# Performance work log

Measured on AMD Instinct MI355X. Metric: run time of the kernel, lower is better.

The kernel has to match this reference:

```python
import jax, jax.numpy as jnp
import numpy as np

EPS = 1e-5  # torch LayerNorm default


def _ln(x, w, b):
    m = jnp.mean(x, axis=-1, keepdims=True)
    v = jnp.mean((x - m) ** 2, axis=-1, keepdims=True)
    return (x - m) / jnp.sqrt(v + EPS) * w + b


def _conv1x1(x, w, b):
    # x: [B,C,H,W], w: [O,C], b: [O]
    return jnp.einsum('bchw,oc->bohw', x, w) + b[None, :, None, None]


def setup_inputs() -> dict:
    key = jax.random.key(0)
    ks = jax.random.split(key, 5)
    B, Cin, H, W = 8, 384, 64, 64
    D, N = 128, 512
    s = lambda k, shape, scale=0.02: jax.random.normal(k, shape, jnp.float32) * scale
    return {
        'x': jax.random.normal(ks[0], (B, Cin, H, W), jnp.float32),
        'DR': jax.random.normal(ks[1], (N, D), jnp.float32),
        'conv_in_w': s(ks[2], (D, Cin)),
        'conv_in_b': jnp.zeros((D,), jnp.float32),
        'sem_w': s(ks[3], (D, D)),
        'sem_b': jnp.zeros((D,), jnp.float32),
        'norm1_w': jnp.ones((D,), jnp.float32),
        'norm1_b': jnp.zeros((D,), jnp.float32),
        'norm2_w': jnp.ones((D,), jnp.float32),
        'norm2_b': jnp.zeros((D,), jnp.float32),
        'conv_out_w': s(ks[4], (Cin, D)),
        'conv_out_b': jnp.zeros((Cin,), jnp.float32),
    }


def reference(x, DR, conv_in_w, conv_in_b, sem_w, sem_b, norm1_w, norm1_b,
              norm2_w, norm2_b, conv_out_w, conv_out_b):
    B, _, H, W = x.shape
    N = DR.shape[0]
    x_align = _conv1x1(x, conv_in_w, conv_in_b)                      # [B,D,H,W]
    x_sem = _conv1x1(x_align, sem_w, sem_b)                          # semantic_extra (1x1 conv)
    x_sem = x_sem.transpose(0, 2, 3, 1).reshape(B, H * W, -1)        # [B,HW,D]
    x_sem = _ln(x_sem, norm1_w, norm1_b)
    dr = _ln(DR, norm2_w, norm2_b).T                                 # [D,N] (same for all batches)
    # NOTE: original applies norm_1 TWICE for the numerator (faithful quirk)
    c_u = jnp.einsum('bld,dn->bln', _ln(x_sem, norm1_w, norm1_b), dr)  # [B,HW,N]
    c_d_l = jnp.sqrt(jnp.sum(x_sem ** 2, axis=-1, keepdims=True))      # [B,HW,1]
    c_d_r = jnp.sqrt(jnp.sum(dr ** 2, axis=0, keepdims=True))[None]    # [1,1,N]
    sim = c_u / (c_d_l * c_d_r)
    sim_soft = jax.nn.softmax(sim, axis=-1)                          # [B,HW,N]
    sim2d = sim_soft.transpose(0, 2, 1).reshape(B, N, H, W)
    degrad = jnp.einsum('bln,dn->bdl', sim_soft, dr).reshape(B, -1, H, W)  # [B,D,H,W]
    # pow-mask with per-batch min-max normalization
    mask_v = jnp.max(sim2d ** 3, axis=1, keepdims=True)              # [B,1,H,W]
    mn = jnp.min(mask_v.reshape(B, -1), axis=1).reshape(B, 1, 1, 1)
    mx = jnp.max(mask_v.reshape(B, -1), axis=1).reshape(B, 1, 1, 1)
    mask_v = 1.0 - (mask_v - mn) / (mx - mn)
    # topk row selection (torch fancy indexing gives [B,B,K,N]; squeeze(1) is a no-op for B>1)
    max_values = jnp.max(sim_soft, axis=2)                           # [B,HW]
    K = (H * W) // 50
    _, top_idx = jax.lax.top_k(max_values, K)                        # [B,K]
    results = jnp.take(sim_soft, top_idx, axis=1)                    # [B,B,K,N]
    out_img = _conv1x1(degrad, conv_out_w, conv_out_b)               # [B,Cin,H,W]
    return (mask_v, out_img, results)
```

## Files before the change

kernel.cpp:

```cpp
#include <hip/hip_runtime.h>
#include <cstdint>

#define EPS 1e-5f
#define BB   8
#define CIN  384
#define HWs  4096
#define LT   32768
#define DD   128
#define NN   512
#define TOPK 81

typedef short short8 __attribute__((ext_vector_type(8)));
typedef float f32x4  __attribute__((ext_vector_type(4)));

__device__ __forceinline__ unsigned short f2bf(float x) {
  unsigned u = __float_as_uint(x);
  u += 0x7fffu + ((u >> 16) & 1u);
  return (unsigned short)(u >> 16);
}
__device__ __forceinline__ float bf2f(unsigned u16) {
  return __uint_as_float(u16 << 16);
}
__device__ __forceinline__ void put_frag(unsigned short* buf, int tile, int rc, int k, float v) {
  int ks = k >> 5, g = (k >> 3) & 3, j = k & 7;
  int basehw = ((tile * 4 + ks) * 2) * 512 + (g * 16 + rc) * 8 + j;
  unsigned short hi = f2bf(v);
  buf[basehw] = hi;
  buf[basehw + 512] = f2bf(v - bf2f(hi));
}

__global__ __launch_bounds__(64) void k_dr(const float* __restrict__ DR,
    const float* __restrict__ w2, const float* __restrict__ b2,
    const float* __restrict__ w1, const float* __restrict__ b1,
    unsigned short* __restrict__ drwF, unsigned short* __restrict__ drlnF,
    float* __restrict__ t2, float* __restrict__ rcr) {
  int n = blockIdx.x;
  int lane = threadIdx.x;
  const float* row = DR + n * DD;
  float x0 = row[lane], x1 = row[lane + 64];
  float s = x0 + x1, sq = x0 * x0 + x1 * x1;
  #pragma unroll
  for (int o = 32; o; o >>= 1) { s += __shfl_xor(s, o); sq += __shfl_xor(sq, o); }
  float m = s * (1.f / 128.f);
  float v = sq * (1.f / 128.f) - m * m;
  float inv = rsqrtf(v + EPS);
  float y0 = (x0 - m) * inv * w2[lane] + b2[lane];
  float y1 = (x1 - m) * inv * w2[lane + 64] + b2[lane + 64];
  int nt = n >> 4, cc = n & 15;
  put_frag(drwF, nt, cc, lane, y0 * w1[lane]);
  put_frag(drwF, nt, cc, lane + 64, y1 * w1[lane + 64]);
  int ks = n >> 5, gB = (n >> 3) & 3, j = n & 7;
  {
    int d = lane;
    unsigned short hi = f2bf(y0);
    int base = (((d >> 4) * 16 + ks) * 2) * 512 + (gB * 16 + (d & 15)) * 8 + j;
    drlnF[base] = hi;
    drlnF[base + 512] = f2bf(y0 - bf2f(hi));
  }
  {
    int d = lane + 64;
    unsigned short hi = f2bf(y1);
    int base = (((d >> 4) * 16 + ks) * 2) * 512 + (gB * 16 + (d & 15)) * 8 + j;
    drlnF[base] = hi;
    drlnF[base + 512] = f2bf(y1 - bf2f(hi));
  }
  float pt2 = y0 * b1[lane] + y1 * b1[lane + 64];
  float pss = y0 * y0 + y1 * y1;
  #pragma unroll
  for (int o = 32; o; o >>= 1) { pt2 += __shfl_xor(pt2, o); pss += __shfl_xor(pss, o); }
  if (lane == 0) { t2[n] = pt2; rcr[n] = rsqrtf(pss); }
}

__global__ __launch_bounds__(256) void k_bprep(const float* __restrict__ src,
                                               unsigned short* __restrict__ dst,
                                               int K) {
  int rt = blockIdx.x, kb = blockIdx.y;
  int t = threadIdx.x, m = t >> 4, kg = t & 15;
  int k0 = kb * 128 + kg * 8;
  const float* s = src + (size_t)(rt * 16 + m) * K + k0;
  float4 f0 = *(const float4*)s;
  float4 f1 = *(const float4*)(s + 4);
  float vs[8] = {f0.x, f0.y, f0.z, f0.w, f1.x, f1.y, f1.z, f1.w};
  short8 hi, lo;
  #pragma unroll
  for (int j = 0; j < 8; ++j) {
    unsigned short h = f2bf(vs[j]);
    hi[j] = (short)h;
    lo[j] = (short)f2bf(vs[j] - bf2f(h));
  }
  int nkt = K >> 5;
  int ks = k0 >> 5, g = (k0 >> 3) & 3;
  short8* D8 = (short8*)dst;
  int base = ((rt * nkt + ks) * 2) * 64 + g * 16 + m;
  D8[base] = hi;
  D8[base + 64] = lo;
}

__global__ __launch_bounds__(256) void k_convin(const float* __restrict__ x,
    const unsigned short* __restrict__ WinF, const float* __restrict__ bias,
    unsigned short* __restrict__ xaF) {
  __shared__ float smem[64 * 132];
  int t = threadIdx.x;
  int w = t >> 6, lane = t & 63, m = lane & 15, g = lane >> 4;
  int l0 = blockIdx.x * 64;
  int b = l0 >> 12, hw0 = l0 & 4095;
  const float* xb = x + (size_t)b * CIN * HWs + hw0;
  const short8* B8 = (const short8*)WinF;
  f32x4 acc[4][2];
  #pragma unroll
  for (int lt = 0; lt < 4; ++lt)
    #pragma unroll
    for (int j2 = 0; j2 < 2; ++j2) acc[lt][j2] = (f32x4){0.f, 0.f, 0.f, 0.f};
  for (int ks = 0; ks < 12; ++ks) {
    short8 ah[4], al[4];
    const float* xc = xb + (size_t)(ks * 32 + g * 8) * HWs;
    #pragma unroll
    for (int lt = 0; lt < 4; ++lt) {
      const float* xcl = xc + lt * 16 + m;
      float v[8];
      #pragma unroll
      for (int j = 0; j < 8; ++j) v[j] = xcl[(size_t)j * HWs];
      #pragma unroll
      for (int j = 0; j < 8; ++j) {
        unsigned short h = f2bf(v[j]);
        ah[lt][j] = (short)h;
        al[lt][j] = (short)f2bf(v[j] - bf2f(h));
      }
    }
    #pragma unroll
    for (int j2 = 0; j2 < 2; ++j2) {
      int dt = w * 2 + j2;
      short8 bh = B8[((dt * 12 + ks) * 2 + 0) * 64 + lane];
      short8 bl = B8[((dt * 12 + ks) * 2 + 1) * 64 + lane];
      #pragma unroll
      for (int lt = 0; lt < 4; ++lt) {
        acc[lt][j2] = __builtin_amdgcn_mfma_f32_16x16x32_bf16(ah[lt], bh, acc[lt][j2], 0, 0, 0);
        acc[lt][j2] = __builtin_amdgcn_mfma_f32_16x16x32_bf16(ah[lt], bl, acc[lt][j2], 0, 0, 0);
        acc[lt][j2] = __builtin_amdgcn_mfma_f32_16x16x32_bf16(al[lt], bh, acc[lt][j2], 0, 0, 0);
      }
    }
  }
  float bia[2] = {bias[w * 32 + m], bias[w * 32 + 16 + m]};
  #pragma unroll
  for (int lt = 0; lt < 4; ++lt)
    #pragma unroll
    for (int j2 = 0; j2 < 2; ++j2)
      #pragma unroll
      for (int r = 0; r < 4; ++r)
        smem[(lt * 16 + g * 4 + r) * 132 + (w * 2 + j2) * 16 + m] = acc[lt][j2][r] + bia[j2];
  __syncthreads();
  short8* X8 = (short8*)xaF;
  #pragma unroll
  for (int it = 0; it < 4; ++it) {
    int idx = it * 256 + t;
    int l = idx & 63, dq = idx >> 6;
    const float* src = &smem[l * 132 + dq * 8];
    float4 f0 = *(const float4*)src;
    float4 f1 = *(const float4*)(src + 4);
    float vs[8] = {f0.x, f0.y, f0.z, f0.w, f1.x, f1.y, f1.z, f1.w};
    short8 hi, lo;
    #pragma unroll
    for (int j = 0; j < 8; ++j) {
      unsigned short h = f2bf(vs[j]);
      hi[j] = (short)h;
      lo[j] = (short)f2bf(vs[j] - bf2f(h));
    }
    int ltg = (l0 + l) >> 4;
    int idx8 = ((ltg * 4 + (dq >> 2)) * 2) * 64 + (dq & 3) * 16 + (l & 15);
    X8[idx8] = hi;
    X8[idx8 + 64] = lo;
  }
}

__global__ __launch_bounds__(256) void k_sem(const unsigned short* __restrict__ xaF,
    const unsigned short* __restrict__ semWF, const float* __restrict__ bias,
    const float* __restrict__ w1, const float* __restrict__ b1,
    unsigned short* __restrict__ ApF, float* __restrict__ rclv) {
  __shared__ float smem[64 * 132];
  __shared__ float sredS[64][4], sredQ[64][4];
  __shared__ float rowM[64], rowI[64];
  int t = threadIdx.x;
  int w = t >> 6, lane = t & 63, m = lane & 15, g = lane >> 4;
  int l0 = blockIdx.x * 64;
  int lt0 = l0 >> 4;
  const short8* A8 = (const short8*)xaF;
  const short8* B8 = (const short8*)semWF;
  f32x4 acc[4][2];
  #pragma unroll
  for (int lt = 0; lt < 4; ++lt)
    #pragma unroll
    for (int j2 = 0; j2 < 2; ++j2) acc[lt][j2] = (f32x4){0.f, 0.f, 0.f, 0.f};
  #pragma unroll
  for (int ks = 0; ks < 4; ++ks) {
    short8 ah[4], al[4];
    #pragma unroll
    for (int lt = 0; lt < 4; ++lt) {
      ah[lt] = A8[(((lt0 + lt) * 4 + ks) * 2 + 0) * 64 + lane];
      al[lt] = A8[(((lt0 + lt) * 4 + ks) * 2 + 1) * 64 + lane];
    }
    #pragma unroll
    for (int j2 = 0; j2 < 2; ++j2) {
      int dt = w * 2 + j2;
      short8 bh = B8[((dt * 4 + ks) * 2 + 0) * 64 + lane];
      short8 bl = B8[((dt * 4 + ks) * 2 + 1) * 64 + lane];
      #pragma unroll
      for (int lt = 0; lt < 4; ++lt) {
        acc[lt][j2] = __builtin_amdgcn_mfma_f32_16x16x32_bf16(ah[lt], bh, acc[lt][j2], 0, 0, 0);
        acc[lt][j2] = __builtin_amdgcn_mfma_f32_16x16x32_bf16(ah[lt], bl, acc[lt][j2], 0, 0, 0);
        acc[lt][j2] = __builtin_amdgcn_mfma_f32_16x16x32_bf16(al[lt], bh, acc[lt][j2], 0, 0, 0);
      }
    }
  }
  float bia[2] = {bias[w * 32 + m], bias[w * 32 + 16 + m]};
  #pragma unroll
  for (int lt = 0; lt < 4; ++lt)
    #pragma unroll
    for (int j2 = 0; j2 < 2; ++j2)
      #pragma unroll
      for (int r = 0; r < 4; ++r) acc[lt][j2][r] += bia[j2];
  float s1[4][4], q1[4][4];
  #pragma unroll
  for (int lt = 0; lt < 4; ++lt)
    #pragma unroll
    for (int r = 0; r < 4; ++r) {
      float a = acc[lt][0][r], b2v = acc[lt][1][r];
      s1[lt][r] = a + b2v;
      q1[lt][r] = a * a + b2v * b2v;
    }
  #pragma unroll
  for (int o = 1; o < 16; o <<= 1)
    #pragma unroll
    for (int lt = 0; lt < 4; ++lt)
      #pragma unroll
      for (int r = 0; r < 4; ++r) {
        s1[lt][r] += __shfl_xor(s1[lt][r], o);
        q1[lt][r] += __shfl_xor(q1[lt][r], o);
      }
  if (m == 0) {
    #pragma unroll
    for (int lt = 0; lt < 4; ++lt)
      #pragma unroll
      for (int r = 0; r < 4; ++r) {
        sredS[lt * 16 + g * 4 + r][w] = s1[lt][r];
        sredQ[lt * 16 + g * 4 + r][w] = q1[lt][r];
      }
  }
  __syncthreads();
  if (t < 64) {
    float S = sredS[t][0] + sredS[t][1] + sredS[t][2] + sredS[t][3];
    float Q = sredQ[t][0] + sredQ[t][1] + sredQ[t][2] + sredQ[t][3];
    float mu = S * (1.f / 128.f);
    float var = Q * (1.f / 128.f) - mu * mu;
    rowM[t] = mu;
    rowI[t] = rsqrtf(var + EPS);
  }
  __syncthreads();
  float w1v[2] = {w1[w * 32 + m], w1[w * 32 + 16 + m]};
  float b1v[2] = {b1[w * 32 + m], b1[w * 32 + 16 + m]};
  #pragma unroll
  for (int lt = 0; lt < 4; ++lt)
    #pragma unroll
    for (int r = 0; r < 4; ++r) {
      float mu = rowM[lt * 16 + g * 4 + r];
      float iv = rowI[lt * 16 + g * 4 + r];
      float y0 = (acc[lt][0][r] - mu) * iv * w1v[0] + b1v[0];
      float y1 = (acc[lt][1][r] - mu) * iv * w1v[1] + b1v[1];
      acc[lt][0][r] = y0; acc[lt][1][r] = y1;
      s1[lt][r] = y0 + y1;
      q1[lt][r] = y0 * y0 + y1 * y1;
    }
  #pragma unroll
  for (int o = 1; o < 16; o <<= 1)
    #pragma unroll
    for (int lt = 0; lt < 4; ++lt)
      #pragma unroll
      for (int r = 0; r < 4; ++r) {
        s1[lt][r] += __shfl_xor(s1[lt][r], o);
        q1[lt][r] += __shfl_xor(q1[lt][r], o);
      }
  if (m == 0) {
    #pragma unroll
    for (int lt = 0; lt < 4; ++lt)
      #pragma unroll
      for (int r = 0; r < 4; ++r) {
        sredS[lt * 16 + g * 4 + r][w] = s1[lt][r];
        sredQ[lt * 16 + g * 4 + r][w] = q1[lt][r];
      }
  }
  __syncthreads();
  if (t < 64) {
    float S = sredS[t][0] + sredS[t][1] + sredS[t][2] + sredS[t][3];
    float Q = sredQ[t][0] + sredQ[t][1] + sredQ[t][2] + sredQ[t][3];
    float m2 = S * (1.f / 128.f);
    float v2 = Q * (1.f / 128.f) - m2 * m2;
    float inv2 = rsqrtf(v2 + EPS);
    float rcl = rsqrtf(Q);
    rowM[t] = m2;
    rowI[t] = inv2 * rcl;
    rclv[l0 + t] = rcl;
  }
  __syncthreads();
  #pragma unroll
  for (int lt = 0; lt < 4; ++lt)
    #pragma unroll
    for (int r = 0; r < 4; ++r) {
      float m2 = rowM[lt * 16 + g * 4 + r];
      float sc = rowI[lt * 16 + g * 4 + r];
      smem[(lt * 16 + g * 4 + r) * 132 + w * 32 + m] = (acc[lt][0][r] - m2) * sc;
      smem[(lt * 16 + g * 4 + r) * 132 + w * 32 + 16 + m] = (acc[lt][1][r] - m2) * sc;
    }
  __syncthreads();
  short8* O8 = (short8*)ApF;
  #pragma unroll
  for (int it = 0; it < 4; ++it) {
    int idx = it * 256 + t;
    int l = idx & 63, dq = idx >> 6;
    const float* src = &smem[l * 132 + dq * 8];
    float4 f0 = *(const float4*)src;
    float4 f1 = *(const float4*)(src + 4);
    float vs[8] = {f0.x, f0.y, f0.z, f0.w, f1.x, f1.y, f1.z, f1.w};
    short8 hi, lo;
    #pragma unroll
    for (int j = 0; j < 8; ++j) {
      unsigned short h = f2bf(vs[j]);
      hi[j] = (short)h;
      lo[j] = (short)f2bf(vs[j] - bf2f(h));
    }
    int ltg = (l0 + l) >> 4;
    int idx8 = ((ltg * 4 + (dq >> 2)) * 2) * 64 + (dq & 3) * 16 + (l & 15);
    O8[idx8] = hi;
    O8[idx8 + 64] = lo;
  }
}

__global__ __launch_bounds__(256) void k_scores(const unsigned short* __restrict__ ApF,
    const unsigned short* __restrict__ drwF, const float* __restrict__ t2g,
    const float* __restrict__ rcrg, const float* __restrict__ rclg,
    unsigned short* __restrict__ pF, float* __restrict__ maxv) {
  __shared__ __align__(16) float sredM[32][4];
  __shared__ __align__(16) float sredS[32][4];
  __shared__ __align__(16) unsigned short plds[32 * 520];
  int t = threadIdx.x;
  int w = t >> 6, lane = t & 63, c = lane & 15, g = lane >> 4;
  int l0 = blockIdx.x * 32;
  int lt0 = blockIdx.x * 2;
  const short8* A8 = (const short8*)ApF;
  const short8* B8 = (const short8*)drwF;
  f32x4 acc[2][8];
  #pragma unroll
  for (int il = 0; il < 2; ++il)
    #pragma unroll
    for (int jn = 0; jn < 8; ++jn) acc[il][jn] = (f32x4){0.f, 0.f, 0.f, 0.f};
  #pragma unroll
  for (int ks = 0; ks < 4; ++ks) {
    short8 ah0 = A8[((lt0 * 4 + ks) * 2 + 0) * 64 + lane];
    short8 al0 = A8[((lt0 * 4 + ks) * 2 + 1) * 64 + lane];
    short8 ah1 = A8[(((lt0 + 1) * 4 + ks) * 2 + 0) * 64 + lane];
    short8 al1 = A8[(((lt0 + 1) * 4 + ks) * 2 + 1) * 64 + lane];
    #pragma unroll
    for (int jn = 0; jn < 8; ++jn) {
      int nt = w * 8 + jn;
      short8 bh = B8[((nt * 4 + ks) * 2 + 0) * 64 + lane];
      short8 bl = B8[((nt * 4 + ks) * 2 + 1) * 64 + lane];
      acc[0][jn] = __builtin_amdgcn_mfma_f32_16x16x32_bf16(ah0, bh, acc[0][jn], 0, 0, 0);
      acc[0][jn] = __builtin_amdgcn_mfma_f32_16x16x32_bf16(ah0, bl, acc[0][jn], 0, 0, 0);
      acc[0][jn] = __builtin_amdgcn_mfma_f32_16x16x32_bf16(al0, bh, acc[0][jn], 0, 0, 0);
      acc[1][jn] = __builtin_amdgcn_mfma_f32_16x16x32_bf16(ah1, bh, acc[1][jn], 0, 0, 0);
      acc[1][jn] = __builtin_amdgcn_mfma_f32_16x16x32_bf16(ah1, bl, acc[1][jn], 0, 0, 0);
      acc[1][jn] = __builtin_amdgcn_mfma_f32_16x16x32_bf16(al1, bh, acc[1][jn], 0, 0, 0);
    }
  }
  float rcrv[8], t2v[8];
  #pragma unroll
  for (int jn = 0; jn < 8; ++jn) {
    int n = w * 128 + jn * 16 + c;
    rcrv[jn] = rcrg[n]; t2v[jn] = t2g[n];
  }
  float rclr[2][4];
  #pragma unroll
  for (int il = 0; il < 2; ++il)
    #pragma unroll
    for (int r = 0; r < 4; ++r)
      rclr[il][r] = rclg[l0 + il * 16 + g * 4 + r];
  float M[2][4];
  #pragma unroll
  for (int il = 0; il < 2; ++il)
    #pragma unroll
    for (int r = 0; r < 4; ++r) M[il][r] = -1e30f;
  #pragma unroll
  for (int il = 0; il < 2; ++il)
    #pragma unroll
    for (int jn = 0; jn < 8; ++jn) {
      f32x4 a = acc[il][jn];
      #pragma unroll
      for (int r = 0; r < 4; ++r) {
        float s = rcrv[jn] * (a[r] + rclr[il][r] * t2v[jn]);
        a[r] = s;
        M[il][r] = fmaxf(M[il][r], s);
      }
      acc[il][jn] = a;
    }
  #pragma unroll
  for (int o = 1; o < 16; o <<= 1)
    #pragma unroll
    for (int il = 0; il < 2; ++il)
      #pragma unroll
      for (int r = 0; r < 4; ++r)
        M[il][r] = fmaxf(M[il][r], __shfl_xor(M[il][r], o));
  if (c == 0) {
    #pragma unroll
    for (int il = 0; il < 2; ++il)
      #pragma unroll
      for (int r = 0; r < 4; ++r)
        sredM[il * 16 + g * 4 + r][w] = M[il][r];
  }
  __syncthreads();
  float Mf[2][4];
  #pragma unroll
  for (int il = 0; il < 2; ++il)
    #pragma unroll
    for (int r = 0; r < 4; ++r) {
      f32x4 mv = *(const f32x4*)(&sredM[il * 16 + g * 4 + r][0]);
      Mf[il][r] = fmaxf(fmaxf(mv[0], mv[1]), fmaxf(mv[2], mv[3]));
    }
  float S[2][4];
  #pragma unroll
  for (int il = 0; il < 2; ++il)
    #pragma unroll
    for (int r = 0; r < 4; ++r) S[il][r] = 0.f;
  #pragma unroll
  for (int il = 0; il < 2; ++il)
    #pragma unroll
    for (int jn = 0; jn < 8; ++jn) {
      f32x4 a = acc[il][jn];
      #pragma unroll
      for (int r = 0; r < 4; ++r) {
        float e = __expf(a[r] - Mf[il][r]);
        a[r] = e;
        S[il][r] += e;
      }
      acc[il][jn] = a;
    }
  #pragma unroll
  for (int o = 1; o < 16; o <<= 1)
    #pragma unroll
    for (int il = 0; il < 2; ++il)
      #pragma unroll
      for (int r = 0; r < 4; ++r)
        S[il][r] += __shfl_xor(S[il][r], o);
  if (c == 0) {
    #pragma unroll
    for (int il = 0; il < 2; ++il)
      #pragma unroll
      for (int r = 0; r < 4; ++r)
        sredS[il * 16 + g * 4 + r][w] = S[il][r];
  }
  __syncthreads();
  float RS[2][4];
  #pragma unroll
  for (int il = 0; il < 2; ++il)
    #pragma unroll
    for (int r = 0; r < 4; ++r) {
      f32x4 sv = *(const f32x4*)(&sredS[il * 16 + g * 4 + r][0]);
      float tot = sv[0] + sv[1] + sv[2] + sv[3];
      RS[il][r] = 1.f / tot;
    }
  if (w == 0 && c == 0) {
    #pragma unroll
    for (int il = 0; il < 2; ++il)
      #pragma unroll
      for (int r = 0; r < 4; ++r)
        maxv[l0 + il * 16 + g * 4 + r] = RS[il][r];
  }
  #pragma unroll
  for (int il = 0; il < 2; ++il)
    #pragma unroll
    for (int jn = 0; jn < 8; ++jn)
      #pragma unroll
      for (int r = 0; r < 4; ++r)
        plds[(il * 16 + g * 4 + r) * 520 + w * 128 + jn * 16 + c] =
            f2bf(acc[il][jn][r] * RS[il][r]);
  __syncthreads();
  short8* P8o = (short8*)pF;
  #pragma unroll
  for (int it = 0; it < 8; ++it) {
    int slot = it * 256 + t;
    int ltl = slot >> 10;
    int ks = (slot >> 6) & 15;
    int gB = (slot >> 4) & 3;
    int mrow = slot & 15;
    int row = ltl * 16 + mrow;
    int n0 = ks * 32 + gB * 8;
    short8 v = *(const short8*)(&plds[row * 520 + n0]);
    P8o[blockIdx.x * 2048 + slot] = v;
  }
}

__global__ __launch_bounds__(256) void k_deg(const unsigned short* __restrict__ pF,
    const unsigned short* __restrict__ drlnF, const unsigned short* __restrict__ WoF,
    const float* __restrict__ bo, float* __restrict__ out_img) {
  __shared__ float smem[64 * 132];
  int t = threadIdx.x;
  int w = t >> 6, lane = t & 63, c = lane & 15, g = lane >> 4;
  int l0 = blockIdx.x * 64;
  int lt0 = l0 >> 4;
  const short8* P8 = (const short8*)pF;
  const short8* D8 = (const short8*)drlnF;
  const short8* W8 = (const short8*)WoF;
  f32x4 acc[4][2];
  #pragma unroll
  for (int lt = 0; lt < 4; ++lt)
    #pragma unroll
    for (int j2 = 0; j2 < 2; ++j2) acc[lt][j2] = (f32x4){0.f, 0.f, 0.f, 0.f};
  for (int ks = 0; ks < 16; ++ks) {
    short8 a0 = P8[((lt0 + 0) * 16 + ks) * 64 + lane];
    short8 a1 = P8[((lt0 + 1) * 16 + ks) * 64 + lane];
    short8 a2 = P8[((lt0 + 2) * 16 + ks) * 64 + lane];
    short8 a3 = P8[((lt0 + 3) * 16 + ks) * 64 + lane];
    #pragma unroll
    for (int j2 = 0; j2 < 2; ++j2) {
      int dt = w * 2 + j2;
      short8 bh = D8[((dt * 16 + ks) * 2 + 0) * 64 + lane];
      short8 bl = D8[((dt * 16 + ks) * 2 + 1) * 64 + lane];
      acc[0][j2] = __builtin_amdgcn_mfma_f32_16x16x32_bf16(a0, bh, acc[0][j2], 0, 0, 0);
      acc[0][j2] = __builtin_amdgcn_mfma_f32_16x16x32_bf16(a0, bl, acc[0][j2], 0, 0, 0);
      acc[1][j2] = __builtin_amdgcn_mfma_f32_16x16x32_bf16(a1, bh, acc[1][j2], 0, 0, 0);
      acc[1][j2] = __builtin_amdgcn_mfma_f32_16x16x32_bf16(a1, bl, acc[1][j2], 0, 0, 0);
      acc[2][j2] = __builtin_amdgcn_mfma_f32_16x16x32_bf16(a2, bh, acc[2][j2], 0, 0, 0);
      acc[2][j2] = __builtin_amdgcn_mfma_f32_16x16x32_bf16(a2, bl, acc[2][j2], 0, 0, 0);
      acc[3][j2] = __builtin_amdgcn_mfma_f32_16x16x32_bf16(a3, bh, acc[3][j2], 0, 0, 0);
      acc[3][j2] = __builtin_amdgcn_mfma_f32_16x16x32_bf16(a3, bl, acc[3][j2], 0, 0, 0);
    }
  }
  #pragma unroll
  for (int lt = 0; lt < 4; ++lt)
    #pragma unroll
    for (int j2 = 0; j2 < 2; ++j2)
      #pragma unroll
      for (int r = 0; r < 4; ++r)
        smem[(lt * 16 + g * 4 + r) * 132 + w * 32 + j2 * 16 + c] = acc[lt][j2][r];
  __syncthreads();
  f32x4 acc2[4][6];
  #pragma unroll
  for (int lt = 0; lt < 4; ++lt)
    #pragma unroll
    for (int ot = 0; ot < 6; ++ot) acc2[lt][ot] = (f32x4){0.f, 0.f, 0.f, 0.f};
  #pragma unroll
  for (int ks2 = 0; ks2 < 4; ++ks2) {
    short8 dh[4];
    #pragma unroll
    for (int lt = 0; lt < 4; ++lt) {
      const float* src = &smem[(lt * 16 + c) * 132 + ks2 * 32 + g * 8];
      float4 f0 = *(const float4*)src;
      float4 f1 = *(const float4*)(src + 4);
      float vs[8] = {f0.x, f0.y, f0.z, f0.w, f1.x, f1.y, f1.z, f1.w};
      #pragma unroll
      for (int j = 0; j < 8; ++j) dh[lt][j] = (short)f2bf(vs[j]);
    }
    #pragma unroll
    for (int ot = 0; ot < 6; ++ot) {
      int otg = w * 6 + ot;
      short8 wh = W8[((otg * 4 + ks2) * 2 + 0) * 64 + lane];
      short8 wl = W8[((otg * 4 + ks2) * 2 + 1) * 64 + lane];
      #pragma unroll
      for (int lt = 0; lt < 4; ++lt) {
        acc2[lt][ot] = __builtin_amdgcn_mfma_f32_16x16x32_bf16(dh[lt], wh, acc2[lt][ot], 0, 0, 0);
        acc2[lt][ot] = __builtin_amdgcn_mfma_f32_16x16x32_bf16(dh[lt], wl, acc2[lt][ot], 0, 0, 0);
      }
    }
  }
  __syncthreads();
  int b = l0 >> 12, hw0 = l0 & 4095;
  float* ob = out_img + (size_t)b * CIN * HWs + hw0;
  float bov[6];
  #pragma unroll
  for (int ot = 0; ot < 6; ++ot) bov[ot] = bo[w * 96 + ot * 16 + c];
  for (int ot = 0; ot < 6; ++ot) {
    #pragma unroll
    for (int lt = 0; lt < 4; ++lt)
      #pragma unroll
      for (int r = 0; r < 4; ++r)
        smem[(lt * 16 + g * 4 + r) * 65 + w * 16 + c] = acc2[lt][ot][r] + bov[ot];
    __syncthreads();
    #pragma unroll
    for (int i = 0; i < 16; ++i) {
      int idx = t + i * 256;
      int o_l = idx >> 6, ll = idx & 63;
      int o = (o_l >> 4) * 96 + ot * 16 + (o_l & 15);
      ob[(size_t)o * HWs + ll] = smem[ll * 65 + o_l];
    }
    __syncthreads();
  }
}

__global__ __launch_bounds__(256) void k_mask(const float* __restrict__ maxv,
                                              float* __restrict__ outm) {
  int b = blockIdx.x, t = threadIdx.x;
  float c[16];
  float mn = 1e30f, mx = -1e30f;
  #pragma unroll
  for (int j = 0; j < 16; ++j) {
    float x = maxv[b * HWs + t + j * 256];
    float cc = x * x * x;
    c[j] = cc;
    mn = fminf(mn, cc); mx = fmaxf(mx, cc);
  }
  #pragma unroll
  for (int o = 32; o; o >>= 1) { mn = fminf(mn, __shfl_xor(mn, o)); mx = fmaxf(mx, __shfl_xor(mx, o)); }
  __shared__ float smn[4], smx[4];
  int w = t >> 6;
  if ((t & 63) == 0) { smn[w] = mn; smx[w] = mx; }
  __syncthreads();
  mn = fminf(fminf(smn[0], smn[1]), fminf(smn[2], smn[3]));
  mx = fmaxf(fmaxf(smx[0], smx[1]), fmaxf(smx[2], smx[3]));
  float sc = 1.f / (mx - mn);
  #pragma unroll
  for (int j = 0; j < 16; ++j)
    outm[b * HWs + t + j * 256] = 1.f - (c[j] - mn) * sc;
}

__global__ __launch_bounds__(256) void k_topk(const float* __restrict__ maxv,
                                              int* __restrict__ tix) {
  __shared__ unsigned int hist[4][256];
  __shared__ unsigned long long slist[TOPK];
  __shared__ unsigned long long bc_prefix;
  __shared__ int bc_need, scount;
  int b = blockIdx.x, t = threadIdx.x;
  int w = t >> 6;
  unsigned long long key[16];
  #pragma unroll
  for (int j = 0; j < 16; ++j) {
    int idx = t + j * 256;
    unsigned int bits = __float_as_uint(maxv[b * HWs + idx]);
    key[j] = ((unsigned long long)bits << 12) | (unsigned)(4095 - idx);
  }
  if (t == 0) { bc_prefix = 0ull; bc_need = TOPK; scount = 0; }
  for (int r = 0; r < 6; ++r) {
    int shift = 40 - 8 * r;
    unsigned int* hflat = (unsigned int*)hist;
    hflat[t] = 0; hflat[t + 256] = 0; hflat[t + 512] = 0; hflat[t + 768] = 0;
    __syncthreads();
    unsigned long long prefix = bc_prefix;
    int bins[16];
    #pragma unroll
    for (int j = 0; j < 16; ++j)
      bins[j] = ((key[j] >> (shift + 8)) == prefix) ? (int)((key[j] >> shift) & 255) : -1;
    #pragma unroll
    for (int j = 0; j < 16; ++j) {
      if (bins[j] >= 0) {
        int cnt = 1;
        #pragma unroll
        for (int j2 = j + 1; j2 < 16; ++j2)
          if (bins[j2] == bins[j]) { bins[j2] = -1; ++cnt; }
        atomicAdd(&hist[w][bins[j]], (unsigned)cnt);
      }
    }
    __syncthreads();
    if (t < 64) {
      int cb[4], s = 0;
      #pragma unroll
      for (int j = 0; j < 4; ++j) {
        int bin = 255 - (t * 4 + j);
        cb[j] = (int)(hist[0][bin] + hist[1][bin] + hist[2][bin] + hist[3][bin]);
        s += cb[j];
      }
      int P = s;
      #pragma unroll
      for (int o = 1; o < 64; o <<= 1) {
        int u = __shfl_up(P, o);
        if (t >= o) P += u;
      }
      int need = bc_need;
      unsigned long long mask = __ballot(P >= need);
      int first = __ffsll((long long)mask) - 1;
      if (t == first) {
        int acc = P - s;
        #pragma unroll
        for (int j = 0; j < 4; ++j) {
          if (acc + cb[j] >= need) {
            bc_prefix = (prefix << 8) | (unsigned)(255 - (t * 4 + j));
            bc_need = need - acc;
            break;
          }
          acc += cb[j];
        }
      }
    }
    __syncthreads();
  }
  unsigned long long K81 = bc_prefix;
  #pragma unroll
  for (int j = 0; j < 16; ++j)
    if (key[j] >= K81) {
      int pos = atomicAdd(&scount, 1);
      slist[pos] = key[j];
    }
  __syncthreads();
  if (t < TOPK) {
    unsigned long long mine = slist[t];
    int rank = 0;
    for (int i = 0; i < TOPK; ++i) rank += (slist[i] > mine) ? 1 : 0;
    tix[b * TOPK + rank] = 4095 - (int)(mine & 0xFFFull);
  }
}

__global__ __launch_bounds__(128) void k_gather(const unsigned short* __restrict__ pF,
    const int* __restrict__ tix, float* __restrict__ outr) {
  int gB_ = blockIdx.x;
  int k = gB_ % TOPK;
  int bb = gB_ / TOPK;
  int b2 = bb & 7, b = bb >> 3;
  int l = b * HWs + tix[b2 * TOPK + k];
  int lt = l >> 4, mrow = l & 15;
  int t = threadIdx.x;
  int ks = t >> 3, gq = (t >> 1) & 3, j0 = (t & 1) * 4;
  int base = ((lt * 16 + ks) * 64 + gq * 16 + mrow) * 8 + j0;
  const unsigned* src = (const unsigned*)(pF + base);
  unsigned u0 = src[0], u1 = src[1];
  float4 v = {bf2f(u0 & 0xffffu), bf2f(u0 >> 16), bf2f(u1 & 0xffffu), bf2f(u1 >> 16)};
  *(float4*)(outr + (size_t)gB_ * NN + t * 4) = v;
}

extern "C" void kernel_launch(void* const* d_in, const int* in_sizes, int n_in,
                              void* d_out, int out_size, void* d_ws, size_t ws_size,
                              hipStream_t stream) {
  const float* x    = (const float*)d_in[0];
  const float* DR   = (const float*)d_in[1];
  const float* win  = (const float*)d_in[2];
  const float* bin  = (const float*)d_in[3];
  const float* sw   = (const float*)d_in[4];
  const float* sb   = (const float*)d_in[5];
  const float* n1w  = (const float*)d_in[6];
  const float* n1b  = (const float*)d_in[7];
  const float* n2w  = (const float*)d_in[8];
  const float* n2b  = (const float*)d_in[9];
  const float* wout = (const float*)d_in[10];
  const float* bout = (const float*)d_in[11];
  float* out = (float*)d_out;
  float* W = (float*)d_ws;

  unsigned short* drwF  = (unsigned short*)(W);
  float* t2   = W + 65536;
  float* rcr  = W + 66048;
  float* rclv = W + 66560;
  float* maxv = W + 99328;
  unsigned short* drlnF = (unsigned short*)(W + 132096);
  unsigned short* WoF   = (unsigned short*)(W + 197632);
  unsigned short* WinF  = (unsigned short*)(W + 246784);
  unsigned short* semWF = (unsigned short*)(W + 295936);
  unsigned short* ApF   = (unsigned short*)(W + 312320);
  unsigned short* xaF   = (unsigned short*)(W + 4506624);
  unsigned short* pF    = (unsigned short*)(W + 4506624);
  int*   tix  = (int*)(W + 12895232);

  float* out_mask = out;
  float* out_img  = out + 32768;
  float* out_res  = out + 32768 + 12582912;

  k_dr    <<<NN, 64, 0, stream>>>(DR, n2w, n2b, n1w, n1b, drwF, drlnF, t2, rcr);
  k_bprep <<<dim3(8, 3),  256, 0, stream>>>(win,  WinF,  CIN);
  k_bprep <<<dim3(8, 1),  256, 0, stream>>>(sw,   semWF, DD);
  k_bprep <<<dim3(24, 1), 256, 0, stream>>>(wout, WoF,   DD);
  k_convin<<<512,  256, 0, stream>>>(x, WinF, bin, xaF);
  k_sem   <<<512,  256, 0, stream>>>(xaF, semWF, sb, n1w, n1b, ApF, rclv);
  k_scores<<<1024, 256, 0, stream>>>(ApF, drwF, t2, rcr, rclv, pF, maxv);
  k_deg   <<<512,  256, 0, stream>>>(pF, drlnF, WoF, bout, out_img);
  k_mask  <<<BB,   256, 0, stream>>>(maxv, out_mask);
  k_topk  <<<BB,   256, 0, stream>>>(maxv, tix);
  k_gather<<<BB * BB * TOPK, 128, 0, stream>>>(pF, tix, out_res);
}
```

Before: 242.5 us.

## Fuse input 1x1 conv and semantic conv+LayerNorm into one kernel

New measurement: 225.9 us. -6.9%, faster.

```diff
diff --git a/kernel.cpp b/kernel.cpp
--- a/kernel.cpp
+++ b/kernel.cpp
@@ -96,35 +96,54 @@
   D8[base + 64] = lo;
 }
 
-__global__ __launch_bounds__(256) void k_convin(const float* __restrict__ x,
-    const unsigned short* __restrict__ WinF, const float* __restrict__ bias,
-    unsigned short* __restrict__ xaF) {
-  __shared__ float smem[64 * 132];
+__global__ __launch_bounds__(256) void k_convsem(const float* __restrict__ x,
+    const unsigned short* __restrict__ WinF, const float* __restrict__ bin,
+    const unsigned short* __restrict__ semWF, const float* __restrict__ sb,
+    const float* __restrict__ w1, const float* __restrict__ b1,
+    unsigned short* __restrict__ ApF, float* __restrict__ rclv) {
+  __shared__ unsigned int shbuf[32 * 132];
+  __shared__ float sredS[32][4], sredQ[32][4];
+  __shared__ float rowM[32], rowI[32];
   int t = threadIdx.x;
   int w = t >> 6, lane = t & 63, m = lane & 15, g = lane >> 4;
-  int l0 = blockIdx.x * 64;
+  int l0 = blockIdx.x * 32;
   int b = l0 >> 12, hw0 = l0 & 4095;
   const float* xb = x + (size_t)b * CIN * HWs + hw0;
   const short8* B8 = (const short8*)WinF;
-  f32x4 acc[4][2];
-  #pragma unroll
-  for (int lt = 0; lt < 4; ++lt)
+  int chs = t & 31, hwo = (t >> 5) * 4;
+  const float* xs = xb + (size_t)chs * HWs + hwo;
+  f32x4 acc[2][2];
+  #pragma unroll
+  for (int lt = 0; lt < 2; ++lt)
     #pragma unroll
     for (int j2 = 0; j2 < 2; ++j2) acc[lt][j2] = (f32x4){0.f, 0.f, 0.f, 0.f};
+  float4 u = *(const float4*)xs;
   for (int ks = 0; ks < 12; ++ks) {
-    short8 ah[4], al[4];
-    const float* xc = xb + (size_t)(ks * 32 + g * 8) * HWs;
-    #pragma unroll
-    for (int lt = 0; lt < 4; ++lt) {
-      const float* xcl = xc + lt * 16 + m;
-      float v[8];
-      #pragma unroll
-      for (int j = 0; j < 8; ++j) v[j] = xcl[(size_t)j * HWs];
-      #pragma unroll
-      for (int j = 0; j < 8; ++j) {
-        unsigned short h = f2bf(v[j]);
-        ah[lt][j] = (short)h;
-        al[lt][j] = (short)f2bf(v[j] - bf2f(h));
+    {
+      float vv[4] = {u.x, u.y, u.z, u.w};
+      #pragma unroll
+      for (int i = 0; i < 4; ++i) {
+        unsigned short h = f2bf(vv[i]);
+        unsigned short lo = f2bf(vv[i] - bf2f(h));
+        shbuf[(hwo + i) * 36 + chs] = (unsigned)h | ((unsigned)lo << 16);
+      }
+    }
+    __syncthreads();
+    if (ks < 11) u = *(const float4*)(xs + (size_t)((ks + 1) * 32) * HWs);
+    short8 ah[2], al[2];
+    #pragma unroll
+    for (int lt = 0; lt < 2; ++lt) {
+      const unsigned* src = &shbuf[(lt * 16 + m) * 36 + g * 8];
+      uint4 p0 = *(const uint4*)(src);
+      uint4 p1 = *(const uint4*)(src + 4);
+      unsigned uu[8] = {p0.x, p0.y, p0.z, p0.w, p1.x, p1.y, p1.z, p1.w};
+      unsigned* ahp = (unsigned*)&ah[lt];
+      unsigned* alp = (unsigned*)&al[lt];
+      #pragma unroll
+      for (int jj = 0; jj < 4; ++jj) {
+        unsigned e0 = uu[2 * jj], e1 = uu[2 * jj + 1];
+        ahp[jj] = (e0 & 0xffffu) | (e1 << 16);
+        alp[jj] = (e0 >> 16) | (e1 & 0xffff0000u);
       }
     }
     #pragma unroll
@@ -133,104 +152,89 @@
       short8 bh = B8[((dt * 12 + ks) * 2 + 0) * 64 + lane];
       short8 bl = B8[((dt * 12 + ks) * 2 + 1) * 64 + lane];
       #pragma unroll
-      for (int lt = 0; lt < 4; ++lt) {
+      for (int lt = 0; lt < 2; ++lt) {
         acc[lt][j2] = __builtin_amdgcn_mfma_f32_16x16x32_bf16(ah[lt], bh, acc[lt][j2], 0, 0, 0);
         acc[lt][j2] = __builtin_amdgcn_mfma_f32_16x16x32_bf16(ah[lt], bl, acc[lt][j2], 0, 0, 0);
         acc[lt][j2] = __builtin_amdgcn_mfma_f32_16x16x32_bf16(al[lt], bh, acc[lt][j2], 0, 0, 0);
       }
     }
-  }
-  float bia[2] = {bias[w * 32 + m], bias[w * 32 + 16 + m]};
-  #pragma unroll
-  for (int lt = 0; lt < 4; ++lt)
-    #pragma unroll
-    for (int j2 = 0; j2 < 2; ++j2)
-      #pragma unroll
-      for (int r = 0; r < 4; ++r)
-        smem[(lt * 16 + g * 4 + r) * 132 + (w * 2 + j2) * 16 + m] = acc[lt][j2][r] + bia[j2];
-  __syncthreads();
-  short8* X8 = (short8*)xaF;
-  #pragma unroll
-  for (int it = 0; it < 4; ++it) {
-    int idx = it * 256 + t;
-    int l = idx & 63, dq = idx >> 6;
-    const float* src = &smem[l * 132 + dq * 8];
-    float4 f0 = *(const float4*)src;
-    float4 f1 = *(const float4*)(src + 4);
-    float vs[8] = {f0.x, f0.y, f0.z, f0.w, f1.x, f1.y, f1.z, f1.w};
-    short8 hi, lo;
-    #pragma unroll
-    for (int j = 0; j < 8; ++j) {
-      unsigned short h = f2bf(vs[j]);
-      hi[j] = (short)h;
-      lo[j] = (short)f2bf(vs[j] - bf2f(h));
-    }
-    int ltg = (l0 + l) >> 4;
-    int idx8 = ((ltg * 4 + (dq >> 2)) * 2) * 64 + (dq & 3) * 16 + (l & 15);
-    X8[idx8] = hi;
-    X8[idx8 + 64] = lo;
-  }
-}
-
-__global__ __launch_bounds__(256) void k_sem(const unsigned short* __restrict__ xaF,
-    const unsigned short* __restrict__ semWF, const float* __restrict__ bias,
-    const float* __restrict__ w1, const float* __restrict__ b1,
-    unsigned short* __restrict__ ApF, float* __restrict__ rclv) {
-  __shared__ float smem[64 * 132];
-  __shared__ float sredS[64][4], sredQ[64][4];
-  __shared__ float rowM[64], rowI[64];
-  int t = threadIdx.x;
-  int w = t >> 6, lane = t & 63, m = lane & 15, g = lane >> 4;
-  int l0 = blockIdx.x * 64;
-  int lt0 = l0 >> 4;
-  const short8* A8 = (const short8*)xaF;
-  const short8* B8 = (const short8*)semWF;
-  f32x4 acc[4][2];
-  #pragma unroll
-  for (int lt = 0; lt < 4; ++lt)
-    #pragma unroll
-    for (int j2 = 0; j2 < 2; ++j2) acc[lt][j2] = (f32x4){0.f, 0.f, 0.f, 0.f};
-  #pragma unroll
-  for (int ks = 0; ks < 4; ++ks) {
-    short8 ah[4], al[4];
-    #pragma unroll
-    for (int lt = 0; lt < 4; ++lt) {
-      ah[lt] = A8[(((lt0 + lt) * 4 + ks) * 2 + 0) * 64 + lane];
-      al[lt] = A8[(((lt0 + lt) * 4 + ks) * 2 + 1) * 64 + lane];
+    __syncthreads();
+  }
+  {
+    float bia[2] = {bin[w * 32 + m], bin[w * 32 + 16 + m]};
+    #pragma unroll
+    for (int lt = 0; lt < 2; ++lt)
+      #pragma unroll
+      for (int j2 = 0; j2 < 2; ++j2)
+        #pragma unroll
+        for (int r = 0; r < 4; ++r) {
+          float v = acc[lt][j2][r] + bia[j2];
+          unsigned short h = f2bf(v);
+          unsigned short lo = f2bf(v - bf2f(h));
+          shbuf[(lt * 16 + g * 4 + r) * 132 + (w * 2 + j2) * 16 + m] =
+              (unsigned)h | ((unsigned)lo << 16);
+        }
+  }
+  __syncthreads();
+  const short8* S8 = (const short8*)semWF;
+  f32x4 acc2[2][2];
+  #pragma unroll
+  for (int lt = 0; lt < 2; ++lt)
+    #pragma unroll
+    for (int j2 = 0; j2 < 2; ++j2) acc2[lt][j2] = (f32x4){0.f, 0.f, 0.f, 0.f};
+  #pragma unroll
+  for (int ks2 = 0; ks2 < 4; ++ks2) {
+    short8 ah2[2], al2[2];
+    #pragma unroll
+    for (int lt = 0; lt < 2; ++lt) {
+      const unsigned* src = &shbuf[(lt * 16 + m) * 132 + ks2 * 32 + g * 8];
+      uint4 p0 = *(const uint4*)(src);
+      uint4 p1 = *(const uint4*)(src + 4);
+      unsigned uu[8] = {p0.x, p0.y, p0.z, p0.w, p1.x, p1.y, p1.z, p1.w};
+      unsigned* ahp = (unsigned*)&ah2[lt];
+      unsigned* alp = (unsigned*)&al2[lt];
+      #pragma unroll
+      for (int jj = 0; jj < 4; ++jj) {
+        unsigned e0 = uu[2 * jj], e1 = uu[2 * jj + 1];
+        ahp[jj] = (e0 & 0xffffu) | (e1 << 16);
+        alp[jj] = (e0 >> 16) | (e1 & 0xffff0000u);
+      }
     }
     #pragma unroll
     for (int j2 = 0; j2 < 2; ++j2) {
       int dt = w * 2 + j2;
-      short8 bh = B8[((dt * 4 + ks) * 2 + 0) * 64 + lane];
-      short8 bl = B8[((dt * 4 + ks) * 2 + 1) * 64 + lane];
-      #pragma unroll
-      for (int lt = 0; lt < 4; ++lt) {
-        acc[lt][j2] = __builtin_amdgcn_mfma_f32_16x16x32_bf16(ah[lt], bh, acc[lt][j2], 0, 0, 0);
-        acc[lt][j2] = __builtin_amdgcn_mfma_f32_16x16x32_bf16(ah[lt], bl, acc[lt][j2], 0, 0, 0);
-        acc[lt][j2] = __builtin_amdgcn_mfma_f32_16x16x32_bf16(al[lt], bh, acc[lt][j2], 0, 0, 0);
-      }
-    }
-  }
-  float bia[2] = {bias[w * 32 + m], bias[w * 32 + 16 + m]};
-  #pragma unroll
-  for (int lt = 0; lt < 4; ++lt)
-    #pragma unroll
-    for (int j2 = 0; j2 < 2; ++j2)
-      #pragma unroll
-      for (int r = 0; r < 4; ++r) acc[lt][j2][r] += bia[j2];
-  float s1[4][4], q1[4][4];
-  #pragma unroll
-  for (int lt = 0; lt < 4; ++lt)
+      short8 bh = S8[((dt * 4 + ks2) * 2 + 0) * 64 + lane];
+      short8 bl = S8[((dt * 4 + ks2) * 2 + 1) * 64 + lane];
+      #pragma unroll
+      for (int lt = 0; lt < 2; ++lt) {
+        acc2[lt][j2] = __builtin_amdgcn_mfma_f32_16x16x32_bf16(ah2[lt], bh, acc2[lt][j2], 0, 0, 0);
+        acc2[lt][j2] = __builtin_amdgcn_mfma_f32_16x16x32_bf16(ah2[lt], bl, acc2[lt][j2], 0, 0, 0);
+        acc2[lt][j2] = __builtin_amdgcn_mfma_f32_16x16x32_bf16(al2[lt], bh, acc2[lt][j2], 0, 0, 0);
+      }
+    }
+  }
+  {
+    float bia2[2] = {sb[w * 32 + m], sb[w * 32 + 16 + m]};
+    #pragma unroll
+    for (int lt = 0; lt < 2; ++lt)
+      #pragma unroll
+      for (int j2 = 0; j2 < 2; ++j2)
+        #pragma unroll
+        for (int r = 0; r < 4; ++r) acc2[lt][j2][r] += bia2[j2];
+  }
+  float s1[2][4], q1[2][4];
+  #pragma unroll
+  for (int lt = 0; lt < 2; ++lt)
     #pragma unroll
     for (int r = 0; r < 4; ++r) {
-      float a = acc[lt][0][r], b2v = acc[lt][1][r];
+      float a = acc2[lt][0][r], b2v = acc2[lt][1][r];
       s1[lt][r] = a + b2v;
       q1[lt][r] = a * a + b2v * b2v;
     }
   #pragma unroll
   for (int o = 1; o < 16; o <<= 1)
     #pragma unroll
-    for (int lt = 0; lt < 4; ++lt)
+    for (int lt = 0; lt < 2; ++lt)
       #pragma unroll
       for (int r = 0; r < 4; ++r) {
         s1[lt][r] += __shfl_xor(s1[lt][r], o);
@@ -238,7 +242,7 @@
       }
   if (m == 0) {
     #pragma unroll
-    for (int lt = 0; lt < 4; ++lt)
+    for (int lt = 0; lt < 2; ++lt)
       #pragma unroll
       for (int r = 0; r < 4; ++r) {
         sredS[lt * 16 + g * 4 + r][w] = s1[lt][r];
@@ -246,7 +250,7 @@
       }
   }
   __syncthreads();
-  if (t < 64) {
+  if (t < 32) {
     float S = sredS[t][0] + sredS[t][1] + sredS[t][2] + sredS[t][3];
     float Q = sredQ[t][0] + sredQ[t][1] + sredQ[t][2] + sredQ[t][3];
     float mu = S * (1.f / 128.f);
@@ -258,21 +262,21 @@
   float w1v[2] = {w1[w * 32 + m], w1[w * 32 + 16 + m]};
   float b1v[2] = {b1[w * 32 + m], b1[w * 32 + 16 + m]};
   #pragma unroll
-  for (int lt = 0; lt < 4; ++lt)
+  for (int lt = 0; lt < 2; ++lt)
     #pragma unroll
     for (int r = 0; r < 4; ++r) {
       float mu = rowM[lt * 16 + g * 4 + r];
       float iv = rowI[lt * 16 + g * 4 + r];
-      float y0 = (acc[lt][0][r] - mu) * iv * w1v[0] + b1v[0];
-      float y1 = (acc[lt][1][r] - mu) * iv * w1v[1] + b1v[1];
-      acc[lt][0][r] = y0; acc[lt][1][r] = y1;
+      float y0 = (acc2[lt][0][r] - mu) * iv * w1v[0] + b1v[0];
+      float y1 = (acc2[lt][1][r] - mu) * iv * w1v[1] + b1v[1];
+      acc2[lt][0][r] = y0; acc2[lt][1][r] = y1;
       s1[lt][r] = y0 + y1;
       q1[lt][r] = y0 * y0 + y1 * y1;
     }
   #pragma unroll
   for (int o = 1; o < 16; o <<= 1)
     #pragma unroll
-    for (int lt = 0; lt < 4; ++lt)
+    for (int lt = 0; lt < 2; ++lt)
       #pragma unroll
       for (int r = 0; r < 4; ++r) {
         s1[lt][r] += __shfl_xor(s1[lt][r], o);
@@ -280,7 +284,7 @@
       }
   if (m == 0) {
     #pragma unroll
-    for (int lt = 0; lt < 4; ++lt)
+    for (int lt = 0; lt < 2; ++lt)
       #pragma unroll
       for (int r = 0; r < 4; ++r) {
         sredS[lt * 16 + g * 4 + r][w] = s1[lt][r];
@@ -288,7 +292,7 @@
       }
   }
   __syncthreads();
-  if (t < 64) {
+  if (t < 32) {
     float S = sredS[t][0] + sredS[t][1] + sredS[t][2] + sredS[t][3];
     float Q = sredQ[t][0] + sredQ[t][1] + sredQ[t][2] + sredQ[t][3];
     float m2 = S * (1.f / 128.f);
@@ -300,22 +304,23 @@
     rclv[l0 + t] = rcl;
   }
   __syncthreads();
-  #pragma unroll
-  for (int lt = 0; lt < 4; ++lt)
+  float* smemf = (float*)shbuf;
+  #pragma unroll
+  for (int lt = 0; lt < 2; ++lt)
     #pragma unroll
     for (int r = 0; r < 4; ++r) {
       float m2 = rowM[lt * 16 + g * 4 + r];
       float sc = rowI[lt * 16 + g * 4 + r];
-      smem[(lt * 16 + g * 4 + r) * 132 + w * 32 + m] = (acc[lt][0][r] - m2) * sc;
-      smem[(lt * 16 + g * 4 + r) * 132 + w * 32 + 16 + m] = (acc[lt][1][r] - m2) * sc;
+      smemf[(lt * 16 + g * 4 + r) * 132 + w * 32 + m] = (acc2[lt][0][r] - m2) * sc;
+      smemf[(lt * 16 + g * 4 + r) * 132 + w * 32 + 16 + m] = (acc2[lt][1][r] - m2) * sc;
     }
   __syncthreads();
   short8* O8 = (short8*)ApF;
   #pragma unroll
-  for (int it = 0; it < 4; ++it) {
+  for (int it = 0; it < 2; ++it) {
     int idx = it * 256 + t;
-    int l = idx & 63, dq = idx >> 6;
-    const float* src = &smem[l * 132 + dq * 8];
+    int l = idx & 31, dq = idx >> 5;
+    const float* src = &smemf[l * 132 + dq * 8];
     float4 f0 = *(const float4*)src;
     float4 f1 = *(const float4*)(src + 4);
     float vs[8] = {f0.x, f0.y, f0.z, f0.w, f1.x, f1.y, f1.z, f1.w};
@@ -749,7 +754,6 @@
   unsigned short* WinF  = (unsigned short*)(W + 246784);
   unsigned short* semWF = (unsigned short*)(W + 295936);
   unsigned short* ApF   = (unsigned short*)(W + 312320);
-  unsigned short* xaF   = (unsigned short*)(W + 4506624);
   unsigned short* pF    = (unsigned short*)(W + 4506624);
   int*   tix  = (int*)(W + 12895232);
 
@@ -757,15 +761,14 @@
   float* out_img  = out + 32768;
   float* out_res  = out + 32768 + 12582912;
 
-  k_dr    <<<NN, 64, 0, stream>>>(DR, n2w, n2b, n1w, n1b, drwF, drlnF, t2, rcr);
-  k_bprep <<<dim3(8, 3),  256, 0, stream>>>(win,  WinF,  CIN);
-  k_bprep <<<dim3(8, 1),  256, 0, stream>>>(sw,   semWF, DD);
-  k_bprep <<<dim3(24, 1), 256, 0, stream>>>(wout, WoF,   DD);
-  k_convin<<<512,  256, 0, stream>>>(x, WinF, bin, xaF);
-  k_sem   <<<512,  256, 0, stream>>>(xaF, semWF, sb, n1w, n1b, ApF, rclv);
-  k_scores<<<1024, 256, 0, stream>>>(ApF, drwF, t2, rcr, rclv, pF, maxv);
-  k_deg   <<<512,  256, 0, stream>>>(pF, drlnF, WoF, bout, out_img);
-  k_mask  <<<BB,   256, 0, stream>>>(maxv, out_mask);
-  k_topk  <<<BB,   256, 0, stream>>>(maxv, tix);
-  k_gather<<<BB * BB * TOPK, 128, 0, stream>>>(pF, tix, out_res);
-}
+  k_dr     <<<NN, 64, 0, stream>>>(DR, n2w, n2b, n1w, n1b, drwF, drlnF, t2, rcr);
+  k_bprep  <<<dim3(8, 3),  256, 0, stream>>>(win,  WinF,  CIN);
+  k_bprep  <<<dim3(8, 1),  256, 0, stream>>>(sw,   semWF, DD);
+  k_bprep  <<<dim3(24, 1), 256, 0, stream>>>(wout, WoF,   DD);
+  k_convsem<<<1024, 256, 0, stream>>>(x, WinF, bin, semWF, sb, n1w, n1b, ApF, rclv);
+  k_scores <<<1024, 256, 0, stream>>>(ApF, drwF, t2, rcr, rclv, pF, maxv);
+  k_deg    <<<512,  256, 0, stream>>>(pF, drlnF, WoF, bout, out_img);
+  k_mask   <<<BB,   256, 0, stream>>>(maxv, out_mask);
+  k_topk   <<<BB,   256, 0, stream>>>(maxv, tix);
+  k_gather <<<BB * BB * TOPK, 128, 0, stream>>>(pF, tix, out_res);
+}
```
